# Kernel optimization log

Hardware: AMD Instinct MI355X
Metric: run time of the kernel (lower is better)

Reference implementation:

```python
import jax, jax.numpy as jnp
import numpy as np

EN_HID = 1024
DE_HID = 1024
BATCH = 64
SRC_LEN = 2048


def setup_inputs() -> dict:
    key = jax.random.key(0)
    ks = jax.random.split(key, 7)
    s_en = 1.0 / np.sqrt(EN_HID)
    s_de = 1.0 / np.sqrt(DE_HID)
    return {
        "hidden": jax.random.normal(ks[0], (1, BATCH, DE_HID), jnp.float32),
        "en_output": jax.random.normal(ks[1], (BATCH, SRC_LEN, EN_HID), jnp.float32),
        "w_en_w": jax.random.uniform(ks[2], (DE_HID, EN_HID), jnp.float32, -s_en, s_en),
        "w_en_b": jax.random.uniform(ks[3], (DE_HID,), jnp.float32, -s_en, s_en),
        "w_de_w": jax.random.uniform(ks[4], (DE_HID, DE_HID), jnp.float32, -s_de, s_de),
        "w_de_b": jax.random.uniform(ks[5], (DE_HID,), jnp.float32, -s_de, s_de),
        "v_w": jax.random.uniform(ks[6], (1, DE_HID), jnp.float32, -s_de, s_de),
    }


def reference(hidden, en_output, w_en_w, w_en_b, w_de_w, w_de_b, v_w):
    # hidden: (1, B, Dd) -> (B, 1, Dd); broadcast over src_len instead of repeat
    h = jnp.transpose(hidden, (1, 0, 2))  # (B, 1, Dd)
    proj_en = jnp.einsum('bse,de->bsd', en_output, w_en_w) + w_en_b  # (B, S, Dd)
    proj_de = jnp.einsum('bqh,dh->bqd', h, w_de_w) + w_de_b          # (B, 1, Dd)
    energy = jnp.tanh(proj_en + proj_de)                              # (B, S, Dd)
    scores = jnp.einsum('bsd,od->bs', energy, v_w)                   # (B, S)
    attention = jax.nn.softmax(scores, axis=1)                        # (B, S)
    weighted = jnp.einsum('bs,bse->be', attention, en_output)[:, None, :]  # (B, 1, E)
    return weighted, attention
```

## Files before the change

kernel.cpp:

```cpp
#include <hip/hip_runtime.h>
#include <stdint.h>

typedef __attribute__((ext_vector_type(4))) float  f32x4;
typedef __attribute__((ext_vector_type(8))) short  bf16x8;

#define BATCH   64
#define SRC_LEN 2048
#define HID     1024
#define M_TOT   (BATCH*SRC_LEN)

#define BM 256
#define BN 256
#define BK 64
#define NT (HID/BK)

__device__ __forceinline__ short f2bf(float f) {
  unsigned u = __builtin_bit_cast(unsigned, f);
  u += 0x7fffu + ((u >> 16) & 1u);
  return (short)(u >> 16);
}

__global__ void k_convert_w(const float* __restrict__ w, short* __restrict__ wb) {
  int i = (blockIdx.x * 256 + threadIdx.x) * 8;
  f32x4 a = *(const f32x4*)(w + i);
  f32x4 b = *(const f32x4*)(w + i + 4);
  bf16x8 o;
  o[0]=f2bf(a[0]); o[1]=f2bf(a[1]); o[2]=f2bf(a[2]); o[3]=f2bf(a[3]);
  o[4]=f2bf(b[0]); o[5]=f2bf(b[1]); o[6]=f2bf(b[2]); o[7]=f2bf(b[3]);
  *(bf16x8*)(wb + i) = o;
}

__global__ void k_convert_en(const float* __restrict__ in, short* __restrict__ out) {
  size_t stride = (size_t)gridDim.x * 256 * 8;
  size_t base = ((size_t)blockIdx.x * 256 + threadIdx.x) * 8;
  size_t total = (size_t)M_TOT * HID;
  for (; base < total; base += stride) {
    f32x4 a = *(const f32x4*)(in + base);
    f32x4 b = *(const f32x4*)(in + base + 4);
    bf16x8 o;
    o[0]=f2bf(a[0]); o[1]=f2bf(a[1]); o[2]=f2bf(a[2]); o[3]=f2bf(a[3]);
    o[4]=f2bf(b[0]); o[5]=f2bf(b[1]); o[6]=f2bf(b[2]); o[7]=f2bf(b[3]);
    *(bf16x8*)(out + base) = o;
  }
}

__global__ void k_bias(const float* __restrict__ hidden, const float* __restrict__ w_de_w,
                       const float* __restrict__ w_en_b, const float* __restrict__ w_de_b,
                       float* __restrict__ bias_all) {
  __shared__ float hid[HID];
  int b  = blockIdx.x >> 2;
  int dc = blockIdx.x & 3;
  for (int i = threadIdx.x; i < HID; i += 256) hid[i] = hidden[b*HID + i];
  __syncthreads();
  int d = dc*256 + threadIdx.x;
  const f32x4* wrow = (const f32x4*)(w_de_w + (size_t)d*HID);
  float acc = 0.f;
  #pragma unroll 8
  for (int q = 0; q < HID/4; ++q) {
    f32x4 w4 = wrow[q];
    f32x4 h4 = *(const f32x4*)&hid[q*4];
    acc += w4[0]*h4[0] + w4[1]*h4[1] + w4[2]*h4[2] + w4[3]*h4[3];
  }
  bias_all[b*HID + d] = acc + w_en_b[d] + w_de_b[d];
}

__global__ void __launch_bounds__(512, 2) k_gemm_score_fast(
    const short* __restrict__ Abf,
    const short* __restrict__ Bw,
    const float* __restrict__ bias_all,
    const float* __restrict__ v_w,
    float* __restrict__ scores)
{
  __shared__ short As[2][BM][BK];
  __shared__ short Bs[2][BN][BK];

  int raw  = blockIdx.x;
  int xcd  = raw & 7;
  int idx  = raw >> 3;
  int mblk = xcd * 64 + (idx >> 2);
  int nblk = idx & 3;
  int m0 = mblk * BM, n0 = nblk * BN;

  int tid  = threadIdx.x;
  int lane = tid & 63;
  int wid  = tid >> 6;
  int wm = wid >> 2, wn = wid & 3;
  int fr  = lane & 15;
  int fko = (lane >> 4) * 8;
  int rsw = (fr & 7) << 3;

  f32x4 acc[8][4] = {};

  auto stage = [&](int buf, int kt) {
    #pragma unroll
    for (int q = 0; q < 4; ++q) {
      int c = q*512 + tid;
      int r = c >> 3;
      int s = (c & 7) ^ (r & 7);
      const short* srcA = Abf + (size_t)(m0 + r) * HID + kt*BK + s*8;
      __builtin_amdgcn_global_load_lds(
          (const __attribute__((address_space(1))) void*)srcA,
          (__attribute__((address_space(3))) void*)((char*)&As[buf][0][0] + c*16),
          16, 0, 0);
    }
    #pragma unroll
    for (int q = 0; q < 4; ++q) {
      int c = q*512 + tid;
      int r = c >> 3;
      int s = (c & 7) ^ (r & 7);
      const short* srcB = Bw + (size_t)(n0 + r) * HID + kt*BK + s*8;
      __builtin_amdgcn_global_load_lds(
          (const __attribute__((address_space(1))) void*)srcB,
          (__attribute__((address_space(3))) void*)((char*)&Bs[buf][0][0] + c*16),
          16, 0, 0);
    }
  };

  auto compute = [&](int buf) {
    bf16x8 aF[8], bF[4];
    #define LDA(mq) { _Pragma("unroll") for (int mi = 0; mi < 4; ++mi) \
        _Pragma("unroll") for (int kk = 0; kk < 2; ++kk) \
          aF[mi*2+kk] = *(const bf16x8*)&As[buf][wm*128 + (mq)*64 + mi*16 + fr][(kk*32 + fko) ^ rsw]; }
    #define LDB(nq) { _Pragma("unroll") for (int ni = 0; ni < 2; ++ni) \
        _Pragma("unroll") for (int kk = 0; kk < 2; ++kk) \
          bF[ni*2+kk] = *(const bf16x8*)&Bs[buf][wn*64 + (nq)*32 + ni*16 + fr][(kk*32 + fko) ^ rsw]; }
    #define MM(mq,nq) { __builtin_amdgcn_s_setprio(1); \
        _Pragma("unroll") for (int mi = 0; mi < 4; ++mi) \
        _Pragma("unroll") for (int ni = 0; ni < 2; ++ni) \
        _Pragma("unroll") for (int kk = 0; kk < 2; ++kk) \
          acc[(mq)*4+mi][(nq)*2+ni] = __builtin_amdgcn_mfma_f32_16x16x32_bf16( \
              aF[mi*2+kk], bF[ni*2+kk], acc[(mq)*4+mi][(nq)*2+ni], 0, 0, 0); \
        __builtin_amdgcn_s_setprio(0); }
    LDA(0); LDB(0); MM(0,0);
    LDB(1);         MM(0,1);
    LDA(1);         MM(1,1);
    LDB(0);         MM(1,0);
    #undef LDA
    #undef LDB
    #undef MM
  };

  stage(0, 0);
  for (int it = 0; it < 8; ++it) {
    stage(1, 2*it + 1);
    asm volatile("s_waitcnt vmcnt(8)" ::: "memory");
    __builtin_amdgcn_s_barrier();
    compute(0);
    asm volatile("s_waitcnt lgkmcnt(0)" ::: "memory");
    __builtin_amdgcn_s_barrier();
    if (it < 7) {
      stage(0, 2*it + 2);
      asm volatile("s_waitcnt vmcnt(8)" ::: "memory");
    } else {
      asm volatile("s_waitcnt vmcnt(0)" ::: "memory");
    }
    __builtin_amdgcn_s_barrier();
    compute(1);
    if (it < 7) {
      asm volatile("s_waitcnt lgkmcnt(0)" ::: "memory");
      __builtin_amdgcn_s_barrier();
    }
  }

  int b = m0 >> 11;
  float vv[4], bb[4];
  #pragma unroll
  for (int nf = 0; nf < 4; ++nf) {
    int col = n0 + wn*64 + nf*16 + fr;
    vv[nf] = v_w[col];
    bb[nf] = bias_all[b*HID + col];
  }
  #pragma unroll
  for (int mf = 0; mf < 8; ++mf) {
    #pragma unroll
    for (int j = 0; j < 4; ++j) {
      float p = 0.f;
      #pragma unroll
      for (int nf = 0; nf < 4; ++nf)
        p += tanhf(acc[mf][nf][j] + bb[nf]) * vv[nf];
      p += __shfl_xor(p, 1);
      p += __shfl_xor(p, 2);
      p += __shfl_xor(p, 4);
      p += __shfl_xor(p, 8);
      if (fr == 0) {
        int row = wm*128 + mf*16 + ((lane >> 4) << 2) + j;
        atomicAdd(&scores[m0 + row], p);
      }
    }
  }
}

__global__ void __launch_bounds__(256) k_gemm_score_conv(
    const float* __restrict__ A, const short* __restrict__ Bw,
    const float* __restrict__ bias_all, const float* __restrict__ v_w,
    float* __restrict__ scores)
{
  __shared__ short Asl[128][64];
  __shared__ short Bsl[128][64];
  int raw  = blockIdx.x;
  int xcd  = raw & 7;
  int idx  = raw >> 3;
  int mblk = xcd * (M_TOT/128/8) + (idx >> 3);
  int nblk = idx & 7;
  int m0 = mblk * 128, n0 = nblk * 128;
  int tid  = threadIdx.x;
  int lane = tid & 63;
  int wid  = tid >> 6;
  int wr = wid >> 1, wc = wid & 1;
  int fr  = lane & 15;
  int fko = (lane >> 4) * 8;
  f32x4 acc[4][4] = {};
  int ar = tid >> 1;
  int ac = (tid & 1) * 32;
  const float* aBase = A + (size_t)(m0 + ar) * HID + ac;
  f32x4 aReg[8];
  #pragma unroll
  for (int i = 0; i < 8; ++i) aReg[i] = *(const f32x4*)(aBase + i*4);
  for (int kt = 0; kt < 16; ++kt) {
    __syncthreads();
    #pragma unroll
    for (int g = 0; g < 4; ++g) {
      bf16x8 w;
      w[0]=f2bf(aReg[2*g][0]);   w[1]=f2bf(aReg[2*g][1]);
      w[2]=f2bf(aReg[2*g][2]);   w[3]=f2bf(aReg[2*g][3]);
      w[4]=f2bf(aReg[2*g+1][0]); w[5]=f2bf(aReg[2*g+1][1]);
      w[6]=f2bf(aReg[2*g+1][2]); w[7]=f2bf(aReg[2*g+1][3]);
      *(bf16x8*)&Asl[ar][ac + g*8] = w;
    }
    #pragma unroll
    for (int j = 0; j < 4; ++j) {
      int c = j*256 + tid;
      const short* src = Bw + (size_t)(n0 + (c >> 3)) * HID + kt*64 + (c & 7)*8;
      __builtin_amdgcn_global_load_lds(
          (const __attribute__((address_space(1))) void*)src,
          (__attribute__((address_space(3))) void*)((char*)&Bsl[0][0] + c*16),
          16, 0, 0);
    }
    __syncthreads();
    if (kt + 1 < 16) {
      const float* nxt = aBase + (kt+1)*64;
      #pragma unroll
      for (int i = 0; i < 8; ++i) aReg[i] = *(const f32x4*)(nxt + i*4);
    }
    #pragma unroll
    for (int kk = 0; kk < 2; ++kk) {
      bf16x8 aF[4], bF[4];
      #pragma unroll
      for (int mi = 0; mi < 4; ++mi)
        aF[mi] = *(const bf16x8*)&Asl[wr*64 + mi*16 + fr][kk*32 + fko];
      #pragma unroll
      for (int ni = 0; ni < 4; ++ni)
        bF[ni] = *(const bf16x8*)&Bsl[wc*64 + ni*16 + fr][kk*32 + fko];
      #pragma unroll
      for (int mi = 0; mi < 4; ++mi)
        #pragma unroll
        for (int ni = 0; ni < 4; ++ni)
          acc[mi][ni] = __builtin_amdgcn_mfma_f32_16x16x32_bf16(aF[mi], bF[ni], acc[mi][ni], 0, 0, 0);
    }
  }
  int b = m0 >> 11;
  float vv[4], bb[4];
  #pragma unroll
  for (int ni = 0; ni < 4; ++ni) {
    int col = n0 + wc*64 + ni*16 + fr;
    vv[ni] = v_w[col];
    bb[ni] = bias_all[b*HID + col];
  }
  #pragma unroll
  for (int mi = 0; mi < 4; ++mi) {
    #pragma unroll
    for (int j = 0; j < 4; ++j) {
      float p = 0.f;
      #pragma unroll
      for (int ni = 0; ni < 4; ++ni)
        p += tanhf(acc[mi][ni][j] + bb[ni]) * vv[ni];
      p += __shfl_xor(p, 1);
      p += __shfl_xor(p, 2);
      p += __shfl_xor(p, 4);
      p += __shfl_xor(p, 8);
      if (fr == 0) {
        int row = wr*64 + mi*16 + ((lane >> 4) << 2) + j;
        atomicAdd(&scores[m0 + row], p);
      }
    }
  }
}

__global__ void k_softmax(float* __restrict__ attn) {
  int b = blockIdx.x;
  float* row = attn + (size_t)b * SRC_LEN;
  int tid = threadIdx.x, lane = tid & 63, wid = tid >> 6;
  __shared__ float red[4];
  float v[8];
  #pragma unroll
  for (int i = 0; i < 8; ++i) v[i] = row[tid + i*256];
  float mx = v[0];
  #pragma unroll
  for (int i = 1; i < 8; ++i) mx = fmaxf(mx, v[i]);
  #pragma unroll
  for (int o = 32; o; o >>= 1) mx = fmaxf(mx, __shfl_xor(mx, o));
  if (lane == 0) red[wid] = mx;
  __syncthreads();
  mx = fmaxf(fmaxf(red[0], red[1]), fmaxf(red[2], red[3]));
  float s = 0.f;
  #pragma unroll
  for (int i = 0; i < 8; ++i) { v[i] = __expf(v[i] - mx); s += v[i]; }
  #pragma unroll
  for (int o = 32; o; o >>= 1) s += __shfl_xor(s, o);
  __syncthreads();
  if (lane == 0) red[wid] = s;
  __syncthreads();
  s = red[0] + red[1] + red[2] + red[3];
  float inv = 1.f / s;
  #pragma unroll
  for (int i = 0; i < 8; ++i) row[tid + i*256] = v[i] * inv;
}

__global__ void k_weighted(const float* __restrict__ en, const float* __restrict__ attn,
                           float* __restrict__ outw) {
  int b  = blockIdx.x >> 4;
  int sc = blockIdx.x & 15;
  __shared__ float aw[128];
  int tid = threadIdx.x;
  if (tid < 128) aw[tid] = attn[b*SRC_LEN + sc*128 + tid];
  __syncthreads();
  const float* base = en + ((size_t)b*SRC_LEN + sc*128) * HID + tid*4;
  f32x4 acc = {0.f, 0.f, 0.f, 0.f};
  #pragma unroll 8
  for (int s = 0; s < 128; ++s) {
    f32x4 x = *(const f32x4*)(base + (size_t)s*HID);
    float w = aw[s];
    acc[0] += w*x[0]; acc[1] += w*x[1]; acc[2] += w*x[2]; acc[3] += w*x[3];
  }
  float* o = outw + b*HID + tid*4;
  atomicAdd(o+0, acc[0]); atomicAdd(o+1, acc[1]);
  atomicAdd(o+2, acc[2]); atomicAdd(o+3, acc[3]);
}

extern "C" void kernel_launch(void* const* d_in, const int* in_sizes, int n_in,
                              void* d_out, int out_size, void* d_ws, size_t ws_size,
                              hipStream_t stream) {
  const float* hidden = (const float*)d_in[0];
  const float* en     = (const float*)d_in[1];
  const float* w_en_w = (const float*)d_in[2];
  const float* w_en_b = (const float*)d_in[3];
  const float* w_de_w = (const float*)d_in[4];
  const float* w_de_b = (const float*)d_in[5];
  const float* v_w    = (const float*)d_in[6];

  float* outw = (float*)d_out;
  float* attn = outw + BATCH*HID;

  const size_t en_elems = (size_t)M_TOT * HID;
  const size_t need_fast = en_elems*sizeof(short) + (size_t)HID*HID*sizeof(short)
                         + (size_t)BATCH*HID*sizeof(float);

  hipMemsetAsync(d_out, 0, (size_t)out_size * sizeof(float), stream);

  if (ws_size >= need_fast) {
    short* en_bf    = (short*)d_ws;
    short* w_bf     = en_bf + en_elems;
    float* bias_all = (float*)(w_bf + (size_t)HID*HID);

    k_convert_en<<<dim3(2048), dim3(256), 0, stream>>>(en, en_bf);
    k_convert_w<<<dim3(HID*HID/(256*8)), dim3(256), 0, stream>>>(w_en_w, w_bf);
    k_bias<<<dim3(BATCH*4), dim3(256), 0, stream>>>(hidden, w_de_w, w_en_b, w_de_b, bias_all);
    k_gemm_score_fast<<<dim3((M_TOT/BM)*(HID/BN)), dim3(512), 0, stream>>>(en_bf, w_bf, bias_all, v_w, attn);
  } else {
    short* w_bf     = (short*)d_ws;
    float* bias_all = (float*)((char*)d_ws + (size_t)HID*HID*sizeof(short));
    k_convert_w<<<dim3(HID*HID/(256*8)), dim3(256), 0, stream>>>(w_en_w, w_bf);
    k_bias<<<dim3(BATCH*4), dim3(256), 0, stream>>>(hidden, w_de_w, w_en_b, w_de_b, bias_all);
    k_gemm_score_conv<<<dim3((M_TOT/128)*(HID/128)), dim3(256), 0, stream>>>(en, w_bf, bias_all, v_w, attn);
  }

  k_softmax<<<dim3(BATCH), dim3(256), 0, stream>>>(attn);
  k_weighted<<<dim3(BATCH*16), dim3(256), 0, stream>>>(en, attn, outw);
}
```

Measured before the change: 691.1 us.

## Interleave global-to-LDS staging with MFMA sub-tiles in an 8-wave ping-pong schedule

Replaces the coarse stage-then-compute double buffer with a fine-grained schedule. Each K tile is split into four MFMA quadrants, and each quadrant issues part of the next tile's global_load_lds before its matrix ops run. Barriers, waitcnts and sched_barriers separate the phases. Source offsets are precomputed once instead of per stage. The aim is to overlap memory traffic with MFMA more evenly, at the cost of many more barriers and a riskier hand-tuned vmcnt bookkeeping.

```diff
diff --git a/kernel.cpp b/kernel.cpp
--- a/kernel.cpp
+++ b/kernel.cpp
@@ -12,7 +12,6 @@
 #define BM 256
 #define BN 256
 #define BK 64
-#define NT (HID/BK)
 
 __device__ __forceinline__ short f2bf(float f) {
   unsigned u = __builtin_bit_cast(unsigned, f);
@@ -91,76 +90,89 @@
 
   f32x4 acc[8][4] = {};
 
-  auto stage = [&](int buf, int kt) {
-    #pragma unroll
-    for (int q = 0; q < 4; ++q) {
-      int c = q*512 + tid;
-      int r = c >> 3;
-      int s = (c & 7) ^ (r & 7);
-      const short* srcA = Abf + (size_t)(m0 + r) * HID + kt*BK + s*8;
-      __builtin_amdgcn_global_load_lds(
-          (const __attribute__((address_space(1))) void*)srcA,
-          (__attribute__((address_space(3))) void*)((char*)&As[buf][0][0] + c*16),
-          16, 0, 0);
-    }
-    #pragma unroll
-    for (int q = 0; q < 4; ++q) {
-      int c = q*512 + tid;
-      int r = c >> 3;
-      int s = (c & 7) ^ (r & 7);
-      const short* srcB = Bw + (size_t)(n0 + r) * HID + kt*BK + s*8;
-      __builtin_amdgcn_global_load_lds(
-          (const __attribute__((address_space(1))) void*)srcB,
-          (__attribute__((address_space(3))) void*)((char*)&Bs[buf][0][0] + c*16),
-          16, 0, 0);
-    }
-  };
-
-  auto compute = [&](int buf) {
-    bf16x8 aF[8], bF[4];
-    #define LDA(mq) { _Pragma("unroll") for (int mi = 0; mi < 4; ++mi) \
-        _Pragma("unroll") for (int kk = 0; kk < 2; ++kk) \
-          aF[mi*2+kk] = *(const bf16x8*)&As[buf][wm*128 + (mq)*64 + mi*16 + fr][(kk*32 + fko) ^ rsw]; }
-    #define LDB(nq) { _Pragma("unroll") for (int ni = 0; ni < 2; ++ni) \
-        _Pragma("unroll") for (int kk = 0; kk < 2; ++kk) \
-          bF[ni*2+kk] = *(const bf16x8*)&Bs[buf][wn*64 + (nq)*32 + ni*16 + fr][(kk*32 + fko) ^ rsw]; }
-    #define MM(mq,nq) { __builtin_amdgcn_s_setprio(1); \
-        _Pragma("unroll") for (int mi = 0; mi < 4; ++mi) \
-        _Pragma("unroll") for (int ni = 0; ni < 2; ++ni) \
-        _Pragma("unroll") for (int kk = 0; kk < 2; ++kk) \
-          acc[(mq)*4+mi][(nq)*2+ni] = __builtin_amdgcn_mfma_f32_16x16x32_bf16( \
-              aF[mi*2+kk], bF[ni*2+kk], acc[(mq)*4+mi][(nq)*2+ni], 0, 0, 0); \
-        __builtin_amdgcn_s_setprio(0); }
-    LDA(0); LDB(0); MM(0,0);
-    LDB(1);         MM(0,1);
-    LDA(1);         MM(1,1);
-    LDB(0);         MM(1,0);
-    #undef LDA
-    #undef LDB
-    #undef MM
-  };
-
-  stage(0, 0);
+  int cA0 = tid,        cA1 = tid + 1024;
+  int cA2 = tid + 512,  cA3 = tid + 1536;
+  int gb  = ((tid >> 8) << 9) + (tid & 255);
+  int cB0 = gb,         cB1 = gb + 1024;
+  int cB2 = gb + 256,   cB3 = gb + 1280;
+
+  #define SOFF(c, rb) ((size_t)((rb) + ((c) >> 3)) * HID + (size_t)((((c) & 7) ^ (((c) >> 3) & 7)) * 8))
+  const size_t sA0 = SOFF(cA0, m0), sA1 = SOFF(cA1, m0), sA2 = SOFF(cA2, m0), sA3 = SOFF(cA3, m0);
+  const size_t sB0 = SOFF(cB0, n0), sB1 = SOFF(cB1, n0), sB2 = SOFF(cB2, n0), sB3 = SOFF(cB3, n0);
+  #undef SOFF
+
+  #define GLD(SRCP, LDSBASE, DOFF) __builtin_amdgcn_global_load_lds( \
+      (const __attribute__((address_space(1))) void*)(SRCP), \
+      (__attribute__((address_space(3))) void*)((char*)(LDSBASE) + (DOFF)), 16, 0, 0)
+
+  #define STG_A01(OTH, KT) do{ GLD(Abf + sA0 + (KT)*64, &As[OTH][0][0], cA0*16); \
+                               GLD(Abf + sA1 + (KT)*64, &As[OTH][0][0], cA1*16); }while(0)
+  #define STG_A23(OTH, KT) do{ GLD(Abf + sA2 + (KT)*64, &As[OTH][0][0], cA2*16); \
+                               GLD(Abf + sA3 + (KT)*64, &As[OTH][0][0], cA3*16); }while(0)
+  #define STG_B01(OTH, KT) do{ GLD(Bw  + sB0 + (KT)*64, &Bs[OTH][0][0], cB0*16); \
+                               GLD(Bw  + sB1 + (KT)*64, &Bs[OTH][0][0], cB1*16); }while(0)
+  #define STG_B23(OTH, KT) do{ GLD(Bw  + sB2 + (KT)*64, &Bs[OTH][0][0], cB2*16); \
+                               GLD(Bw  + sB3 + (KT)*64, &Bs[OTH][0][0], cB3*16); }while(0)
+
+  bf16x8 aF[8], bF[4];
+  #define LDA(BUF, MQ) { _Pragma("unroll") for (int mi = 0; mi < 4; ++mi) \
+      _Pragma("unroll") for (int kk = 0; kk < 2; ++kk) \
+        aF[mi*2+kk] = *(const bf16x8*)&As[BUF][wm*128 + (MQ)*64 + mi*16 + fr][(kk*32 + fko) ^ rsw]; }
+  #define LDB(BUF, NQ) { _Pragma("unroll") for (int ni = 0; ni < 2; ++ni) \
+      _Pragma("unroll") for (int kk = 0; kk < 2; ++kk) \
+        bF[ni*2+kk] = *(const bf16x8*)&Bs[BUF][wn*64 + (NQ)*32 + ni*16 + fr][(kk*32 + fko) ^ rsw]; }
+  #define MMQ(MQ, NQ) { _Pragma("unroll") for (int mi = 0; mi < 4; ++mi) \
+      _Pragma("unroll") for (int ni = 0; ni < 2; ++ni) \
+      _Pragma("unroll") for (int kk = 0; kk < 2; ++kk) \
+        acc[(MQ)*4+mi][(NQ)*2+ni] = __builtin_amdgcn_mfma_f32_16x16x32_bf16( \
+            aF[mi*2+kk], bF[ni*2+kk], acc[(MQ)*4+mi][(NQ)*2+ni], 0, 0, 0); }
+
+  #define BARR   __builtin_amdgcn_s_barrier()
+  #define LG0    asm volatile("s_waitcnt lgkmcnt(0)" ::: "memory")
+  #define SCHED0 __builtin_amdgcn_sched_barrier(0)
+  #define VMC(N) asm volatile("s_waitcnt vmcnt(" #N ")" ::: "memory")
+  #define PR1    __builtin_amdgcn_s_setprio(1)
+  #define PR0    __builtin_amdgcn_s_setprio(0)
+
+  #define KTILE(BUF, OTH, KT, LAST) do{ \
+     \
+    LDA(BUF, 0); LDB(BUF, 0); \
+    if (!(LAST)) STG_A01(OTH, (KT)+1); \
+    BARR; LG0; SCHED0; PR1; MMQ(0,0); PR0; \
+    if (!(LAST)) { VMC(4); } else { VMC(2); } \
+    BARR; \
+     \
+    LDB(BUF, 1); \
+    if (!(LAST)) STG_B01(OTH, (KT)+1); \
+    BARR; LG0; SCHED0; PR1; MMQ(0,1); PR0; \
+    if (!(LAST)) { VMC(4); } else { VMC(0); } \
+    BARR; \
+     \
+    LDA(BUF, 1); \
+    if (!(LAST)) STG_B23(OTH, (KT)+1); \
+    BARR; LG0; SCHED0; PR1; MMQ(1,1); PR0; BARR; \
+     \
+    LDB(BUF, 0); \
+    if (!(LAST)) STG_A23(OTH, (KT)+1); \
+    BARR; LG0; SCHED0; PR1; MMQ(1,0); PR0; \
+    if (!(LAST)) { VMC(4); } \
+    BARR; \
+  }while(0)
+
+  STG_A01(0, 0); STG_B01(0, 0); STG_B23(0, 0); STG_A23(0, 0);
+  VMC(4); BARR;
+
+  #pragma unroll 1
   for (int it = 0; it < 8; ++it) {
-    stage(1, 2*it + 1);
-    asm volatile("s_waitcnt vmcnt(8)" ::: "memory");
-    __builtin_amdgcn_s_barrier();
-    compute(0);
-    asm volatile("s_waitcnt lgkmcnt(0)" ::: "memory");
-    __builtin_amdgcn_s_barrier();
-    if (it < 7) {
-      stage(0, 2*it + 2);
-      asm volatile("s_waitcnt vmcnt(8)" ::: "memory");
-    } else {
-      asm volatile("s_waitcnt vmcnt(0)" ::: "memory");
-    }
-    __builtin_amdgcn_s_barrier();
-    compute(1);
-    if (it < 7) {
-      asm volatile("s_waitcnt lgkmcnt(0)" ::: "memory");
-      __builtin_amdgcn_s_barrier();
-    }
-  }
+    KTILE(0, 1, 2*it, false);
+    if (it < 7) { KTILE(1, 0, 2*it + 1, false); }
+    else        { KTILE(1, 0, 15,       true ); }
+  }
+
+  #undef KTILE
+  #undef LDA
+  #undef LDB
+  #undef MMQ
 
   int b = m0 >> 11;
   float vv[4], bb[4];
```

After: 1.578 ms. +128.4%, slower.
